# Kernel optimization log

Measured on AMD Instinct MI355X. Metric: run time of the kernel, lower is better.

The kernel has to match this reference:

```python
import jax, jax.numpy as jnp
import numpy as np

E = 1024        # embed_dim
NH = 16         # num_heads
HD = E // NH    # head_dim = 64
MLP = 4096
HID = int(2 * MLP / 3)  # 2730, TransNeXt ConvGLU hidden
NT = 1          # no_rope task tokens (skip rotary / skip dwconv)
B, S = 8, 1025
GRID = 32       # sqrt(S - NT)
EPS = 1e-6
SCALE = HD ** -0.5


def rmsnorm(x, g):
    return x * jax.lax.rsqrt(jnp.mean(x * x, axis=-1, keepdims=True) + EPS) * g


def apply_rope(t):
    # t: [B, NH, s, HD] -- rotate-half RoPE over image-token positions
    s = t.shape[2]
    pos = jnp.arange(s, dtype=jnp.float32)
    inv_freq = 1.0 / (10000.0 ** (jnp.arange(0, HD, 2, dtype=jnp.float32) / HD))
    freqs = pos[:, None] * inv_freq[None, :]          # [s, HD/2]
    cos = jnp.concatenate([jnp.cos(freqs)] * 2, -1)   # [s, HD]
    sin = jnp.concatenate([jnp.sin(freqs)] * 2, -1)
    t1, t2 = jnp.split(t, 2, axis=-1)
    rot = jnp.concatenate([-t2, t1], axis=-1)
    return t * cos + rot * sin


def rope_skip_task(t):
    # first NT tokens are task tokens -> identity; rest get rotary with positions 0..
    return jnp.concatenate([t[:, :, :NT], apply_rope(t[:, :, NT:])], axis=2)


def setup_inputs() -> dict:
    key = jax.random.key(0)
    ks = jax.random.split(key, 12)
    init = lambda k, shape, fan: (jax.random.normal(k, shape, jnp.float32) * (fan ** -0.5))
    return {
        "x": jax.random.normal(ks[0], (B, S, E), jnp.float32),
        "g1": jnp.ones((E,), jnp.float32),
        "w_qkv": init(ks[1], (E, 3 * E), E),
        "b_qkv": jnp.zeros((3 * E,), jnp.float32),
        "w_proj": init(ks[2], (E, E), E),
        "b_proj": jnp.zeros((E,), jnp.float32),
        "g2": jnp.ones((E,), jnp.float32),
        "fc1_w": init(ks[3], (E, 2 * HID), E),
        "fc1_b": jnp.zeros((2 * HID,), jnp.float32),
        "dw_w": init(ks[4], (3, 3, 1, HID), 9),  # HWIO depthwise 3x3
        "dw_b": jnp.zeros((HID,), jnp.float32),
        "fc2_w": init(ks[5], (HID, E), HID),
        "fc2_b": jnp.zeros((E,), jnp.float32),
    }


def reference(x, g1, w_qkv, b_qkv, w_proj, b_proj, g2, fc1_w, fc1_b, dw_w, dw_b, fc2_w, fc2_b):
    # ---- attention block ----
    residual = x
    xn = rmsnorm(x, g1)
    qkv = xn @ w_qkv + b_qkv                              # [B,S,3E]
    qkv = qkv.reshape(B, S, 3, NH, HD).transpose(2, 0, 3, 1, 4)
    q, k, v = qkv[0], qkv[1], qkv[2]                      # [B,NH,S,HD]
    q = rope_skip_task(q)
    k = rope_skip_task(k)
    attn = jnp.einsum("bhqd,bhkd->bhqk", q * SCALE, k)    # [B,NH,S,S]
    attn = jax.nn.softmax(attn, axis=-1)
    out = jnp.einsum("bhqk,bhkd->bhqd", attn, v)          # [B,NH,S,HD]
    out = out.transpose(0, 2, 1, 3).reshape(B, S, E)
    out = out @ w_proj + b_proj
    x = residual + out

    # ---- ConvGLU MLP block ----
    residual = x
    xn = rmsnorm(x, g2)
    h = xn @ fc1_w + fc1_b                                # [B,S,2*HID]
    xg, vg = jnp.split(h, 2, axis=-1)
    x_task, x_img = xg[:, :NT], xg[:, NT:]                # dwconv only on image tokens
    img = x_img.reshape(B, GRID, GRID, HID)
    img = jax.lax.conv_general_dilated(
        img, dw_w, window_strides=(1, 1), padding="SAME",
        feature_group_count=HID,
        dimension_numbers=("NHWC", "HWIO", "NHWC")) + dw_b
    x_img = img.reshape(B, GRID * GRID, HID)
    xc = jnp.concatenate([x_task, x_img], axis=1)
    h = jax.nn.gelu(xc, approximate=False) * vg           # GLU gate
    h = h @ fc2_w + fc2_b
    return residual + h
```

## Files before the change

kernel.cpp:

```cpp
#include <hip/hip_runtime.h>
#include <hip/hip_bf16.h>
#include <math.h>

#define E_DIM 1024
#define NHEAD 16
#define HID_DIM 2730
#define KP_FC2 2752
#define HB_LD 5504
#define XG_OFF 2752
#define FC1_N 5482
#define B_DIM 8
#define S_DIM 1025
#define EPS_V 1e-6f
#define SCALE_V 0.125f
#define MROWS (B_DIM * S_DIM)

typedef __attribute__((ext_vector_type(8))) short short8;
typedef __attribute__((ext_vector_type(4))) float f32x4;
typedef unsigned short us;

__device__ __forceinline__ float b2f(us u) {
    union { unsigned int i; float f; } x; x.i = ((unsigned int)u) << 16; return x.f;
}
__device__ __forceinline__ us f2b(float f) {
    __hip_bfloat16 h = __float2bfloat16(f);
    return *reinterpret_cast<us*>(&h);
}

__device__ __forceinline__ void stage16(const void* g, void* l) {
    __builtin_amdgcn_global_load_lds(
        (const __attribute__((address_space(1))) unsigned int*)g,
        (__attribute__((address_space(3))) unsigned int*)l,
        16, 0, 0);
}

__device__ __forceinline__ int sl(int row, int c8) {
    return (row * 8 + (c8 ^ (row & 7))) * 8;
}

#define MFMA16(a, b, c) __builtin_amdgcn_mfma_f32_16x16x32_bf16(a, b, c, 0, 0, 0)

__global__ __launch_bounds__(256) void rmsnorm_kernel(const float* __restrict__ x,
        const float* __restrict__ g, us* __restrict__ out) {
    int row = blockIdx.x;
    const float4* xr = (const float4*)(x + (size_t)row * E_DIM);
    float4 v = xr[threadIdx.x];
    float ss = v.x*v.x + v.y*v.y + v.z*v.z + v.w*v.w;
    #pragma unroll
    for (int off = 32; off > 0; off >>= 1) ss += __shfl_down(ss, off, 64);
    __shared__ float wsum[4];
    int lane = threadIdx.x & 63, w = threadIdx.x >> 6;
    if (lane == 0) wsum[w] = ss;
    __syncthreads();
    float tot = wsum[0] + wsum[1] + wsum[2] + wsum[3];
    float inv = rsqrtf(tot * (1.0f / E_DIM) + EPS_V);
    float4 gv = ((const float4*)g)[threadIdx.x];
    ushort4 o;
    o.x = f2b(v.x * inv * gv.x); o.y = f2b(v.y * inv * gv.y);
    o.z = f2b(v.z * inv * gv.z); o.w = f2b(v.w * inv * gv.w);
    ((ushort4*)(out + (size_t)row * E_DIM))[threadIdx.x] = o;
}

__global__ __launch_bounds__(256) void convt_kernel(const float* __restrict__ W,
        us* __restrict__ WT, int K, int N, int KPad, int swap_half, int xg_off, int Wld) {
    __shared__ float T[32][33];
    int n0 = blockIdx.x * 32, k0 = blockIdx.y * 32;
    int c = threadIdx.x & 31, r4 = (threadIdx.x >> 5) << 2;
    #pragma unroll
    for (int i = 0; i < 4; i++) {
        int k = k0 + r4 + i, n = n0 + c;
        float v = 0.0f;
        if (k < K && n < N) {
            int src = n;
            int ok = 1;
            if (swap_half) {
                if (n < swap_half) src = n + swap_half;
                else if (xg_off) { if (n >= xg_off) src = n - xg_off; else ok = 0; }
                else src = n - swap_half;
            }
            if (ok) v = W[(size_t)k * Wld + src];
        }
        T[c][r4 + i] = v;
    }
    __syncthreads();
    #pragma unroll
    for (int i = 0; i < 4; i++) {
        int n = n0 + r4 + i, k = k0 + c;
        if (n < N && k < KPad) WT[(size_t)n * KPad + k] = f2b(T[r4 + i][c]);
    }
}

__global__ __launch_bounds__(256) void bias_perm_kernel(const float* __restrict__ b,
        float* __restrict__ bp) {
    int r = blockIdx.x * 256 + threadIdx.x;
    if (r < FC1_N)
        bp[r] = (r < HID_DIM) ? b[r + HID_DIM] : ((r < XG_OFF) ? 0.0f : b[r - XG_OFF]);
}

template<int MODE>
__global__ __launch_bounds__(512, 2) void gemm256(const us* __restrict__ A, int lda,
        const us* __restrict__ Bt, int ldb, const float* __restrict__ bias,
        const float* __restrict__ Rres, void* __restrict__ Cv,
        int M, int N, int K, int ldc, int Ksplit) {
    __shared__ __align__(16) us lds[2][4][8192];
    us* const L = &lds[0][0][0];
    const int tid = threadIdx.x;
    const int lane = tid & 63;
    const int w = tid >> 6;
    const int wm = w >> 2, wn = w & 3;
    const int l15 = lane & 15, quad = lane >> 4;

    const int nwg = gridDim.x * gridDim.y;
    const int orig = blockIdx.y * gridDim.x + blockIdx.x;
    const int q8 = nwg >> 3, r8 = nwg & 7;
    const int xcd = orig & 7, oi = orig >> 3;
    const int wgid = (xcd < r8 ? xcd * (q8 + 1) : r8 * (q8 + 1) + (xcd - r8) * q8) + oi;
    const int m0 = (wgid / gridDim.x) * 256, n0 = (wgid % gridDim.x) * 256;

    const int kz = (MODE == 2) ? (int)blockIdx.z : 0;
    const int kofs = kz * Ksplit;
    const int Keff = (MODE == 2) ? (kz ? K - Ksplit : Ksplit) : K;

    const int r0 = tid >> 3;
    const int c80 = (tid & 7) ^ (r0 & 7);
    const us* const pA = A + (size_t)(m0 + r0) * lda + kofs + c80 * 8;
    const us* const pB = Bt + (size_t)(n0 + r0) * ldb + kofs + c80 * 8;
    const size_t a64 = (size_t)64 * lda, b64 = (size_t)64 * ldb;
    us* const dst = L + tid * 8;

#define STG_A(b, h, kt) do { \
    const us* s_ = pA + (size_t)(h) * 2 * a64 + (size_t)(kt) * 64; \
    stage16(s_,       dst + ((b) * 4 + (h)) * 8192); \
    stage16(s_ + a64, dst + ((b) * 4 + (h)) * 8192 + 4096); \
} while (0)
#define STG_B(b, h, kt) do { \
    const us* s_ = pB + (size_t)(h) * 2 * b64 + (size_t)(kt) * 64; \
    stage16(s_,       dst + ((b) * 4 + 2 + (h)) * 8192); \
    stage16(s_ + b64, dst + ((b) * 4 + 2 + (h)) * 8192 + 4096); \
} while (0)

    f32x4 acc[8][4];
    #pragma unroll
    for (int m = 0; m < 8; m++)
        #pragma unroll
        for (int n = 0; n < 4; n++) acc[m][n] = (f32x4){0.f, 0.f, 0.f, 0.f};

    const int nk = Keff >> 6;
    const int brow = (wn & 1) * 64;

    STG_A(0, 0, 0); STG_A(0, 1, 0);
    STG_B(0, 0, 0); STG_B(0, 1, 0);
    if (nk > 1) {
        STG_B(1, 0, 1); STG_B(1, 1, 1);
        STG_A(1, 0, 1); STG_A(1, 1, 1);
        asm volatile("s_waitcnt vmcnt(8)" ::: "memory");
    } else {
        asm volatile("s_waitcnt vmcnt(0)" ::: "memory");
    }
    __builtin_amdgcn_s_barrier();
    __builtin_amdgcn_sched_barrier(0);

    short8 bf01[2][2];
    {
        const us* bB0 = L + (2 + (wn >> 1)) * 8192;
        #pragma unroll
        for (int n = 0; n < 2; n++) {
            bf01[n][0] = *(const short8*)(bB0 + sl(brow + n * 16 + l15, quad));
            bf01[n][1] = *(const short8*)(bB0 + sl(brow + n * 16 + l15, 4 + quad));
        }
    }

    for (int t = 0; t < nk; t++) {
        const int c = t & 1, cn = c ^ 1;
        const us* aB = L + (c * 4 + wm) * 8192;
        const us* bB = L + (c * 4 + 2 + (wn >> 1)) * 8192;
        const us* bBn = L + (cn * 4 + 2 + (wn >> 1)) * 8192;
        short8 bf2[2][2];
        #pragma unroll
        for (int n = 0; n < 2; n++) {
            bf2[n][0] = *(const short8*)(bB + sl(brow + (n + 2) * 16 + l15, quad));
            bf2[n][1] = *(const short8*)(bB + sl(brow + (n + 2) * 16 + l15, 4 + quad));
        }
        #pragma unroll
        for (int p = 0; p < 4; p++) {
            const int mp = 2 * p;
            short8 a00 = *(const short8*)(aB + sl(mp * 16 + l15, quad));
            short8 a01 = *(const short8*)(aB + sl(mp * 16 + l15, 4 + quad));
            short8 a10 = *(const short8*)(aB + sl(mp * 16 + 16 + l15, quad));
            short8 a11 = *(const short8*)(aB + sl(mp * 16 + 16 + l15, 4 + quad));
            if (p == 1) { if (t + 2 < nk) STG_B(c, 0, t + 2); }
            else if (p == 2) { if (t + 2 < nk) STG_B(c, 1, t + 2); }
            else if (p == 3) {
                if (t + 2 < nk)      { asm volatile("s_waitcnt vmcnt(4)" ::: "memory"); }
                else if (t + 1 < nk) { asm volatile("s_waitcnt vmcnt(0)" ::: "memory"); }
            }
            __builtin_amdgcn_s_barrier();
            if (p == 3) __builtin_amdgcn_sched_barrier(0);
            __builtin_amdgcn_s_setprio(1);
            #pragma unroll
            for (int n = 0; n < 4; n++) {
                const short8 b0 = (n < 2) ? bf01[n][0] : bf2[n - 2][0];
                const short8 b1 = (n < 2) ? bf01[n][1] : bf2[n - 2][1];
                acc[mp][n]     = MFMA16(a00, b0, acc[mp][n]);
                acc[mp][n]     = MFMA16(a01, b1, acc[mp][n]);
                acc[mp + 1][n] = MFMA16(a10, b0, acc[mp + 1][n]);
                acc[mp + 1][n] = MFMA16(a11, b1, acc[mp + 1][n]);
            }
            __builtin_amdgcn_s_setprio(0);
            if (p == 3) {
                if (t + 2 < nk) { STG_A(c, 0, t + 2); STG_A(c, 1, t + 2); }
                if (t + 1 < nk) {
                    #pragma unroll
                    for (int n = 0; n < 2; n++) {
                        bf01[n][0] = *(const short8*)(bBn + sl(brow + n * 16 + l15, quad));
                        bf01[n][1] = *(const short8*)(bBn + sl(brow + n * 16 + l15, 4 + quad));
                    }
                }
            }
            __builtin_amdgcn_s_barrier();
            if (p == 3) __builtin_amdgcn_sched_barrier(0);
        }
    }

    #pragma unroll
    for (int m = 0; m < 8; m++) {
        int gm0 = m0 + wm * 128 + m * 16 + quad * 4;
        #pragma unroll
        for (int n = 0; n < 4; n++) {
            int gn = n0 + wn * 64 + n * 16 + l15;
            if (gn >= N) continue;
            float bs = (MODE == 2) ? (kz == 0 ? bias[gn] : 0.0f) : bias[gn];
            #pragma unroll
            for (int r = 0; r < 4; r++) {
                int gm = gm0 + r;
                if (gm >= M) continue;
                float v = acc[m][n][r] + bs;
                if (MODE == 0) {
                    ((us*)Cv)[(size_t)gm * ldc + gn] = f2b(v);
                } else if (MODE == 1) {
                    ((float*)Cv)[(size_t)gm * ldc + gn] = v + Rres[(size_t)gm * ldc + gn];
                } else {
                    atomicAdd(&((float*)Cv)[(size_t)gm * ldc + gn], v);
                }
            }
        }
    }
#undef STG_A
#undef STG_B
}

__global__ __launch_bounds__(256) void rope_kernel(us* __restrict__ qkv) {
    int idx = blockIdx.x * 256 + threadIdx.x;
    int i = idx & 31;
    int h = (idx >> 5) & (NHEAD - 1);
    int rc = idx >> 9;
    int s = rc % S_DIM;
    us* q = qkv + (size_t)rc * 3072 + h * 64;
    us* k = q + 1024;
    if (s == 0) {
        q[i] = f2b(b2f(q[i]) * SCALE_V);
        q[i + 32] = f2b(b2f(q[i + 32]) * SCALE_V);
        return;
    }
    float pos = (float)(s - 1);
    float invf = expf((float)i * (-9.210340371976184f / 32.0f));
    float f = pos * invf;
    float c = cosf(f), sn = sinf(f);
    float q1 = b2f(q[i]), q2 = b2f(q[i + 32]);
    q[i]      = f2b((q1 * c - q2 * sn) * SCALE_V);
    q[i + 32] = f2b((q2 * c + q1 * sn) * SCALE_V);
    float k1 = b2f(k[i]), k2 = b2f(k[i + 32]);
    k[i]      = f2b(k1 * c - k2 * sn);
    k[i + 32] = f2b(k2 * c + k1 * sn);
}

__global__ __launch_bounds__(256) void vtrans_kernel(const us* __restrict__ qkv,
        us* __restrict__ Vt) {
    __shared__ us T[64][65];
    int st = blockIdx.x, h = blockIdx.y, bc = blockIdx.z;
    int tid = threadIdx.x;
    int r = tid & 63, cb = (tid >> 6) * 16;
    const us* src = qkv + (size_t)(bc * S_DIM + st * 64 + r) * 3072 + 2048 + h * 64 + cb;
    #pragma unroll
    for (int i = 0; i < 4; i++) {
        ushort4 v = *(const ushort4*)(src + i * 4);
        T[cb + i*4 + 0][r] = v.x; T[cb + i*4 + 1][r] = v.y;
        T[cb + i*4 + 2][r] = v.z; T[cb + i*4 + 3][r] = v.w;
    }
    __syncthreads();
    int d = tid >> 2, sc = (tid & 3) * 16;
    us* dstp = Vt + ((size_t)((bc * 16 + h) * 64 + d)) * 1088 + st * 64 + sc;
    #pragma unroll
    for (int g = 0; g < 4; g++) {
        ushort4 o;
        int i0 = sc + g * 4;
        o.x = (st*64 + i0 + 0 < S_DIM) ? T[d][i0 + 0] : 0;
        o.y = (st*64 + i0 + 1 < S_DIM) ? T[d][i0 + 1] : 0;
        o.z = (st*64 + i0 + 2 < S_DIM) ? T[d][i0 + 2] : 0;
        o.w = (st*64 + i0 + 3 < S_DIM) ? T[d][i0 + 3] : 0;
        *(ushort4*)(dstp + g * 4) = o;
    }
}

__global__ __launch_bounds__(256) void attn_kernel(const us* __restrict__ qkv,
        const us* __restrict__ Vt, us* __restrict__ attnb) {
    __shared__ __align__(16) us Kb[2][4096];
    __shared__ __align__(16) us Vb[2][4096];
    __shared__ __align__(16) us Ps[4096];
    int qt = blockIdx.x, h = blockIdx.y, bc = blockIdx.z;
    int tid = threadIdx.x;
    int lane = tid & 63, w = tid >> 6;
    int l15 = lane & 15, quad = lane >> 4;

    const us* qrow = qkv + (size_t)(bc * S_DIM + qt * 64 + 16 * w + l15) * 3072 + h * 64;
    short8 qa0 = *(const short8*)(qrow + quad * 8);
    short8 qa1 = *(const short8*)(qrow + 32 + quad * 8);

    const us* kg = qkv + (size_t)(bc * S_DIM) * 3072 + 1024 + h * 64;
    const us* vgp = Vt + (size_t)((bc * 16 + h) * 64) * 1088;

    int s0 = tid, s1 = 256 + tid;
    int row0 = s0 >> 3, c8_0 = (s0 & 7) ^ (row0 & 7);
    int row1 = s1 >> 3, c8_1 = (s1 & 7) ^ (row1 & 7);

    f32x4 acc_o[4];
    float mr[4], lr[4];
    #pragma unroll
    for (int r = 0; r < 4; r++) { mr[r] = -1e30f; lr[r] = 0.f; }
    #pragma unroll
    for (int j = 0; j < 4; j++) acc_o[j] = (f32x4){0.f, 0.f, 0.f, 0.f};

    stage16(kg + (size_t)row0 * 3072 + c8_0 * 8, Kb[0] + s0 * 8);
    stage16(vgp + (size_t)row0 * 1088 + c8_0 * 8, Vb[0] + s0 * 8);
    stage16(kg + (size_t)row1 * 3072 + c8_1 * 8, Kb[0] + s1 * 8);
    stage16(vgp + (size_t)row1 * 1088 + c8_1 * 8, Vb[0] + s1 * 8);
    __syncthreads();

    for (int kt = 0; kt < 17; kt++) {
        int cur = kt & 1, nxt = cur ^ 1;
        if (kt + 1 < 17) {
            stage16(kg + (size_t)((kt + 1) * 64 + row0) * 3072 + c8_0 * 8, Kb[nxt] + s0 * 8);
            stage16(vgp + (size_t)row0 * 1088 + (kt + 1) * 64 + c8_0 * 8, Vb[nxt] + s0 * 8);
            stage16(kg + (size_t)((kt + 1) * 64 + row1) * 3072 + c8_1 * 8, Kb[nxt] + s1 * 8);
            stage16(vgp + (size_t)row1 * 1088 + (kt + 1) * 64 + c8_1 * 8, Vb[nxt] + s1 * 8);
        }

        f32x4 accS[4];
        #pragma unroll
        for (int j = 0; j < 4; j++) accS[j] = (f32x4){0.f, 0.f, 0.f, 0.f};
        __builtin_amdgcn_s_setprio(1);
        #pragma unroll
        for (int j = 0; j < 4; j++) {
            short8 kb0 = *(const short8*)(Kb[cur] + sl(16 * j + l15, quad));
            short8 kb1 = *(const short8*)(Kb[cur] + sl(16 * j + l15, 4 + quad));
            accS[j] = MFMA16(qa0, kb0, accS[j]);
            accS[j] = MFMA16(qa1, kb1, accS[j]);
        }
        __builtin_amdgcn_s_setprio(0);

        #pragma unroll
        for (int j = 0; j < 4; j++) {
            if (kt * 64 + 16 * j + l15 >= S_DIM) {
                #pragma unroll
                for (int r = 0; r < 4; r++) accS[j][r] = -1e30f;
            }
        }

        float tm[4];
        #pragma unroll
        for (int r = 0; r < 4; r++) {
            float t = fmaxf(fmaxf(accS[0][r], accS[1][r]), fmaxf(accS[2][r], accS[3][r]));
            #pragma unroll
            for (int off = 1; off < 16; off <<= 1)
                t = fmaxf(t, __shfl_xor(t, off, 64));
            tm[r] = t;
        }
        int need = (tm[0] > mr[0] + 8.f) || (tm[1] > mr[1] + 8.f) ||
                   (tm[2] > mr[2] + 8.f) || (tm[3] > mr[3] + 8.f);
        if (__any(need)) {
            #pragma unroll
            for (int r = 0; r < 4; r++) {
                float mnew = fmaxf(mr[r], tm[r]);
                float al = __expf(mr[r] - mnew);
                mr[r] = mnew;
                lr[r] *= al;
                #pragma unroll
                for (int j = 0; j < 4; j++) acc_o[j][r] *= al;
            }
        }
        float pr[4][4];
        #pragma unroll
        for (int r = 0; r < 4; r++) {
            float rs = 0.f;
            #pragma unroll
            for (int j = 0; j < 4; j++) {
                float p = __expf(accS[j][r] - mr[r]);
                pr[j][r] = p;
                rs += p;
            }
            lr[r] += rs;
        }
        #pragma unroll
        for (int j = 0; j < 4; j++) {
            #pragma unroll
            for (int r = 0; r < 4; r++) {
                int prow = quad * 4 + r;
                int idx = sl(16 * w + prow, 2 * j + (l15 >> 3)) + (l15 & 7);
                Ps[idx] = f2b(pr[j][r]);
            }
        }
        short8 pa0 = *(const short8*)(Ps + sl(16 * w + l15, quad));
        short8 pa1 = *(const short8*)(Ps + sl(16 * w + l15, 4 + quad));
        __builtin_amdgcn_s_setprio(1);
        #pragma unroll
        for (int j = 0; j < 4; j++) {
            short8 vb0 = *(const short8*)(Vb[cur] + sl(16 * j + l15, quad));
            short8 vb1 = *(const short8*)(Vb[cur] + sl(16 * j + l15, 4 + quad));
            acc_o[j] = MFMA16(pa0, vb0, acc_o[j]);
            acc_o[j] = MFMA16(pa1, vb1, acc_o[j]);
        }
        __builtin_amdgcn_s_setprio(0);
        __syncthreads();
    }

    #pragma unroll
    for (int r = 0; r < 4; r++) {
        #pragma unroll
        for (int off = 1; off < 16; off <<= 1)
            lr[r] += __shfl_xor(lr[r], off, 64);
    }
    #pragma unroll
    for (int r = 0; r < 4; r++) {
        int s = qt * 64 + 16 * w + quad * 4 + r;
        if (s >= S_DIM) continue;
        float invl = 1.0f / lr[r];
        #pragma unroll
        for (int j = 0; j < 4; j++)
            attnb[(size_t)(bc * S_DIM + s) * E_DIM + h * 64 + 16 * j + l15] =
                f2b(acc_o[j][r] * invl);
    }
}

__global__ __launch_bounds__(256) void conv_gelu_kernel(us* __restrict__ hb,
        const float* __restrict__ dw_w, const float* __restrict__ dw_b) {
    int p = blockIdx.x % S_DIM;
    size_t row = blockIdx.x;
    size_t brow = row - p;
    int pp = p - 1;
    int gy = pp >> 5, gx = pp & 31;
    for (int g = threadIdx.x; g < 342; g += 256) {
        int c0 = g * 8;
        if (c0 + 8 <= HID_DIM) {
            float val[8];
            if (p == 0) {
                short8 xv = *(const short8*)(hb + row * HB_LD + XG_OFF + c0);
                #pragma unroll
                for (int e = 0; e < 8; e++) val[e] = b2f((us)xv[e]);
            } else {
                #pragma unroll
                for (int e = 0; e < 8; e++) val[e] = dw_b[c0 + e];
                #pragma unroll
                for (int dy = 0; dy < 3; dy++) {
                    int ny = gy + dy - 1;
                    if (ny < 0 || ny >= 32) continue;
                    #pragma unroll
                    for (int dx = 0; dx < 3; dx++) {
                        int nx = gx + dx - 1;
                        if (nx < 0 || nx >= 32) continue;
                        short8 xv = *(const short8*)(hb +
                                (brow + 1 + ny * 32 + nx) * HB_LD + XG_OFF + c0);
                        const float* wp = dw_w + (dy * 3 + dx) * HID_DIM + c0;
                        float2 w0 = *(const float2*)(wp);
                        float2 w1 = *(const float2*)(wp + 2);
                        float2 w2 = *(const float2*)(wp + 4);
                        float2 w3 = *(const float2*)(wp + 6);
                        val[0] = fmaf(b2f((us)xv[0]), w0.x, val[0]);
                        val[1] = fmaf(b2f((us)xv[1]), w0.y, val[1]);
                        val[2] = fmaf(b2f((us)xv[2]), w1.x, val[2]);
                        val[3] = fmaf(b2f((us)xv[3]), w1.y, val[3]);
                        val[4] = fmaf(b2f((us)xv[4]), w2.x, val[4]);
                        val[5] = fmaf(b2f((us)xv[5]), w2.y, val[5]);
                        val[6] = fmaf(b2f((us)xv[6]), w3.x, val[6]);
                        val[7] = fmaf(b2f((us)xv[7]), w3.y, val[7]);
                    }
                }
            }
            short8 gv = *(const short8*)(hb + row * HB_LD + c0);
            short8 o;
            #pragma unroll
            for (int e = 0; e < 8; e++) {
                float ge = 0.5f * val[e] * (1.0f + erff(val[e] * 0.70710678118654752f));
                o[e] = (short)f2b(ge * b2f((us)gv[e]));
            }
            *(short8*)(hb + row * HB_LD + c0) = o;
        } else {
            for (int c = c0; c < HID_DIM; c++) {
                float val;
                if (p == 0) {
                    val = b2f(hb[row * HB_LD + XG_OFF + c]);
                } else {
                    float a = dw_b[c];
                    #pragma unroll
                    for (int dy = 0; dy < 3; dy++) {
                        int ny = gy + dy - 1;
                        if (ny < 0 || ny >= 32) continue;
                        #pragma unroll
                        for (int dx = 0; dx < 3; dx++) {
                            int nx = gx + dx - 1;
                            if (nx < 0 || nx >= 32) continue;
                            a = fmaf(b2f(hb[(brow + 1 + ny * 32 + nx) * HB_LD + XG_OFF + c]),
                                     dw_w[(dy * 3 + dx) * HID_DIM + c], a);
                        }
                    }
                    val = a;
                }
                float ge = 0.5f * val * (1.0f + erff(val * 0.70710678118654752f));
                hb[row * HB_LD + c] = f2b(ge * b2f(hb[row * HB_LD + c]));
            }
        }
    }
}

static size_t ws_need(int cb) {
    size_t R = (size_t)cb * 1025, Rp = ((R + 127) / 128) * 128;
    size_t end1 = Rp*1024*2 + Rp*3072*2 + (size_t)cb*16*64*1088*2
                + 8320ull*1024*2 + 3072ull*1024*2 + 1024ull*1024*2;
    size_t end2 = Rp*1024*2 + Rp*HB_LD*2 + 5504ull*1024*2 + 1024ull*KP_FC2*2 + 5504*4;
    return end1 > end2 ? end1 : end2;
}

extern "C" void kernel_launch(void* const* d_in, const int* in_sizes, int n_in,
                              void* d_out, int out_size, void* d_ws, size_t ws_size,
                              hipStream_t stream) {
    const float* x      = (const float*)d_in[0];
    const float* g1     = (const float*)d_in[1];
    const float* w_qkv  = (const float*)d_in[2];
    const float* b_qkv  = (const float*)d_in[3];
    const float* w_proj = (const float*)d_in[4];
    const float* b_proj = (const float*)d_in[5];
    const float* g2     = (const float*)d_in[6];
    const float* fc1_w  = (const float*)d_in[7];
    const float* fc1_b  = (const float*)d_in[8];
    const float* dw_w   = (const float*)d_in[9];
    const float* dw_b   = (const float*)d_in[10];
    const float* fc2_w  = (const float*)d_in[11];
    const float* fc2_b  = (const float*)d_in[12];
    float* out = (float*)d_out;
    char* base = (char*)d_ws;

    int CB = 2;
    if (ws_size >= ws_need(8)) CB = 8;
    else if (ws_size >= ws_need(4)) CB = 4;
    int NC = B_DIM / CB;
    size_t R = (size_t)CB * 1025, Rp = ((R + 127) / 128) * 128;
    int gy256 = (int)((R + 255) / 256);

    us* xn    = (us*)base;
    size_t o  = Rp * 1024 * 2;
    us* qkv   = (us*)(base + o);
    us* hbuf  = (us*)(base + o);
    size_t o2 = o + Rp * 3072 * 2;
    us* Vt    = (us*)(base + o2);
    size_t o3 = o2 + (size_t)CB * 16 * 64 * 1088 * 2;
    us* attnb = (us*)(base + o3);
    size_t o4 = o3 + 8320ull * 1024 * 2;
    us* qkvT  = (us*)(base + o4);
    size_t o5 = o4 + 3072ull * 1024 * 2;
    us* projT = (us*)(base + o5);
    size_t p2 = o + Rp * HB_LD * 2;
    us* fc1T  = (us*)(base + p2);
    size_t p3 = p2 + 5504ull * 1024 * 2;
    us* fc2T  = (us*)(base + p3);
    float* fc1bp = (float*)(base + p3 + 1024ull * KP_FC2 * 2);

    convt_kernel<<<dim3(96, 32), 256, 0, stream>>>(w_qkv, qkvT, 1024, 3072, 1024, 0, 0, 3072);
    convt_kernel<<<dim3(32, 32), 256, 0, stream>>>(w_proj, projT, 1024, 1024, 1024, 0, 0, 1024);
    for (int c = 0; c < NC; c++) {
        size_t roff = (size_t)c * R;
        rmsnorm_kernel<<<(int)R, 256, 0, stream>>>(x + roff * E_DIM, g1, xn);
        gemm256<0><<<dim3(12, gy256), 512, 0, stream>>>(xn, 1024, qkvT, 1024,
                b_qkv, nullptr, qkv, (int)R, 3072, 1024, 3072, 0);
        rope_kernel<<<(int)(2 * R), 256, 0, stream>>>(qkv);
        vtrans_kernel<<<dim3(17, 16, CB), 256, 0, stream>>>(qkv, Vt);
        attn_kernel<<<dim3(17, 16, CB), 256, 0, stream>>>(qkv, Vt, attnb + roff * E_DIM);
    }
    gemm256<1><<<dim3(4, (MROWS + 255) / 256), 512, 0, stream>>>(attnb, 1024,
            projT, 1024, b_proj, x, out, MROWS, 1024, 1024, 1024, 0);

    convt_kernel<<<dim3(172, 32), 256, 0, stream>>>(fc1_w, fc1T, 1024, FC1_N, 1024,
            HID_DIM, XG_OFF, 5460);
    convt_kernel<<<dim3(32, 86), 256, 0, stream>>>(fc2_w, fc2T, HID_DIM, 1024, KP_FC2,
            0, 0, 1024);
    bias_perm_kernel<<<22, 256, 0, stream>>>(fc1_b, fc1bp);
    for (int c = 0; c < NC; c++) {
        size_t roff = (size_t)c * R;
        float* outc = out + roff * E_DIM;
        rmsnorm_kernel<<<(int)R, 256, 0, stream>>>(outc, g2, xn);
        gemm256<0><<<dim3(22, gy256), 512, 0, stream>>>(xn, 1024, fc1T, 1024,
                fc1bp, nullptr, hbuf, (int)R, FC1_N, 1024, HB_LD, 0);
        conv_gelu_kernel<<<(int)R, 256, 0, stream>>>(hbuf, dw_w, dw_b);
        gemm256<2><<<dim3(4, gy256, 2), 512, 0, stream>>>(hbuf, HB_LD, fc2T, KP_FC2,
                fc2_b, nullptr, outc, (int)R, 1024, KP_FC2, 1024, 1408);
    }
}
```

Baseline: 814.0 us.

## Replace split-K atomics with partial buffer and fuse reduction into rmsnorm

The split-K GEMM epilogue no longer uses atomicAdd. The first K-half writes the result plus the residual, and the second half writes to a separate fp32 partial buffer. The projection GEMM now also uses split-K, with its partial folded into the following rmsnorm via a new fused add+norm kernel. FC2's partial is added back by a separate add-reduce kernel. This removes atomic traffic and the reliance on pre-initialised output, but adds an extra fp32 buffer plus read/write passes.

Result: faster. 783.1 us (-3.8%).

```diff
diff --git a/kernel.cpp b/kernel.cpp
--- a/kernel.cpp
+++ b/kernel.cpp
@@ -61,6 +61,42 @@
     ((ushort4*)(out + (size_t)row * E_DIM))[threadIdx.x] = o;
 }
 
+__global__ __launch_bounds__(256) void rmsnorm_add_kernel(float* __restrict__ x,
+        const float* __restrict__ p, const float* __restrict__ g, us* __restrict__ out) {
+    int row = blockIdx.x;
+    float4* xr = (float4*)(x + (size_t)row * E_DIM);
+    const float4* pr = (const float4*)(p + (size_t)row * E_DIM);
+    float4 v = xr[threadIdx.x];
+    float4 pv = pr[threadIdx.x];
+    v.x += pv.x; v.y += pv.y; v.z += pv.z; v.w += pv.w;
+    xr[threadIdx.x] = v;
+    float ss = v.x*v.x + v.y*v.y + v.z*v.z + v.w*v.w;
+    #pragma unroll
+    for (int off = 32; off > 0; off >>= 1) ss += __shfl_down(ss, off, 64);
+    __shared__ float wsum[4];
+    int lane = threadIdx.x & 63, w = threadIdx.x >> 6;
+    if (lane == 0) wsum[w] = ss;
+    __syncthreads();
+    float tot = wsum[0] + wsum[1] + wsum[2] + wsum[3];
+    float inv = rsqrtf(tot * (1.0f / E_DIM) + EPS_V);
+    float4 gv = ((const float4*)g)[threadIdx.x];
+    ushort4 o;
+    o.x = f2b(v.x * inv * gv.x); o.y = f2b(v.y * inv * gv.y);
+    o.z = f2b(v.z * inv * gv.z); o.w = f2b(v.w * inv * gv.w);
+    ((ushort4*)(out + (size_t)row * E_DIM))[threadIdx.x] = o;
+}
+
+__global__ __launch_bounds__(256) void addreduce_kernel(float* __restrict__ dst,
+        const float* __restrict__ p, int n4) {
+    int stride = gridDim.x * 256;
+    for (int i = blockIdx.x * 256 + threadIdx.x; i < n4; i += stride) {
+        float4 a = ((const float4*)p)[i];
+        float4 d = ((float4*)dst)[i];
+        d.x += a.x; d.y += a.y; d.z += a.z; d.w += a.w;
+        ((float4*)dst)[i] = d;
+    }
+}
+
 __global__ __launch_bounds__(256) void convt_kernel(const float* __restrict__ W,
         us* __restrict__ WT, int K, int N, int KPad, int swap_half, int xg_off, int Wld) {
     __shared__ float T[32][33];
@@ -101,7 +137,7 @@
 __global__ __launch_bounds__(512, 2) void gemm256(const us* __restrict__ A, int lda,
         const us* __restrict__ Bt, int ldb, const float* __restrict__ bias,
         const float* __restrict__ Rres, void* __restrict__ Cv,
-        int M, int N, int K, int ldc, int Ksplit) {
+        int M, int N, int K, int ldc, int Ksplit, float* __restrict__ Pbuf) {
     __shared__ __align__(16) us lds[2][4][8192];
     us* const L = &lds[0][0][0];
     const int tid = threadIdx.x;
@@ -240,7 +276,10 @@
                 } else if (MODE == 1) {
                     ((float*)Cv)[(size_t)gm * ldc + gn] = v + Rres[(size_t)gm * ldc + gn];
                 } else {
-                    atomicAdd(&((float*)Cv)[(size_t)gm * ldc + gn], v);
+                    if (kz == 0)
+                        ((float*)Cv)[(size_t)gm * ldc + gn] = v + Rres[(size_t)gm * ldc + gn];
+                    else
+                        Pbuf[(size_t)gm * ldc + gn] = v;
                 }
             }
         }
@@ -554,6 +593,12 @@
     int NC = B_DIM / CB;
     size_t R = (size_t)CB * 1025, Rp = ((R + 127) / 128) * 128;
     int gy256 = (int)((R + 255) / 256);
+    int gyM = (MROWS + 255) / 256;
+
+    size_t pOff = ((ws_need(CB) + 255) / 256) * 256;
+    size_t pBytes = (size_t)MROWS * E_DIM * 4;
+    int use_split = (ws_size >= pOff + pBytes);
+    float* P1 = (float*)(base + pOff);
 
     us* xn    = (us*)base;
     size_t o  = Rp * 1024 * 2;
@@ -579,13 +624,18 @@
         size_t roff = (size_t)c * R;
         rmsnorm_kernel<<<(int)R, 256, 0, stream>>>(x + roff * E_DIM, g1, xn);
         gemm256<0><<<dim3(12, gy256), 512, 0, stream>>>(xn, 1024, qkvT, 1024,
-                b_qkv, nullptr, qkv, (int)R, 3072, 1024, 3072, 0);
+                b_qkv, nullptr, qkv, (int)R, 3072, 1024, 3072, 0, nullptr);
         rope_kernel<<<(int)(2 * R), 256, 0, stream>>>(qkv);
         vtrans_kernel<<<dim3(17, 16, CB), 256, 0, stream>>>(qkv, Vt);
         attn_kernel<<<dim3(17, 16, CB), 256, 0, stream>>>(qkv, Vt, attnb + roff * E_DIM);
     }
-    gemm256<1><<<dim3(4, (MROWS + 255) / 256), 512, 0, stream>>>(attnb, 1024,
-            projT, 1024, b_proj, x, out, MROWS, 1024, 1024, 1024, 0);
+    if (use_split) {
+        gemm256<2><<<dim3(4, gyM, 2), 512, 0, stream>>>(attnb, 1024, projT, 1024,
+                b_proj, x, out, MROWS, 1024, 1024, 1024, 512, P1);
+    } else {
+        gemm256<1><<<dim3(4, gyM), 512, 0, stream>>>(attnb, 1024, projT, 1024,
+                b_proj, x, out, MROWS, 1024, 1024, 1024, 0, nullptr);
+    }
 
     convt_kernel<<<dim3(172, 32), 256, 0, stream>>>(fc1_w, fc1T, 1024, FC1_N, 1024,
             HID_DIM, XG_OFF, 5460);
@@ -595,11 +645,22 @@
     for (int c = 0; c < NC; c++) {
         size_t roff = (size_t)c * R;
         float* outc = out + roff * E_DIM;
-        rmsnorm_kernel<<<(int)R, 256, 0, stream>>>(outc, g2, xn);
+        if (use_split) {
+            rmsnorm_add_kernel<<<(int)R, 256, 0, stream>>>(outc, P1 + roff * E_DIM, g2, xn);
+        } else {
+            rmsnorm_kernel<<<(int)R, 256, 0, stream>>>(outc, g2, xn);
+        }
         gemm256<0><<<dim3(22, gy256), 512, 0, stream>>>(xn, 1024, fc1T, 1024,
-                fc1bp, nullptr, hbuf, (int)R, FC1_N, 1024, HB_LD, 0);
+                fc1bp, nullptr, hbuf, (int)R, FC1_N, 1024, HB_LD, 0, nullptr);
         conv_gelu_kernel<<<(int)R, 256, 0, stream>>>(hbuf, dw_w, dw_b);
-        gemm256<2><<<dim3(4, gy256, 2), 512, 0, stream>>>(hbuf, HB_LD, fc2T, KP_FC2,
-                fc2_b, nullptr, outc, (int)R, 1024, KP_FC2, 1024, 1408);
-    }
-}
+        if (use_split) {
+            gemm256<2><<<dim3(4, gy256, 2), 512, 0, stream>>>(hbuf, HB_LD, fc2T, KP_FC2,
+                    fc2_b, outc, outc, (int)R, 1024, KP_FC2, 1024, 1408, P1 + roff * E_DIM);
+            addreduce_kernel<<<2048, 256, 0, stream>>>(outc, P1 + roff * E_DIM,
+                    (int)(R * 256));
+        } else {
+            gemm256<1><<<dim3(4, gy256), 512, 0, stream>>>(hbuf, HB_LD, fc2T, KP_FC2,
+                    fc2_b, outc, outc, (int)R, 1024, KP_FC2, 1024, 0, nullptr);
+        }
+    }
+}
```
